# Kernel tuning notes

Hardware: AMD Instinct MI355X
Metric: run time of the kernel (lower is better)

Reference implementation:

```python
import jax, jax.numpy as jnp
import numpy as np

B, N, C, H = 8, 4096, 768, 12
D = C // H  # head dim = 64


def setup_inputs() -> dict:
    key = jax.random.key(0)
    ks = jax.random.split(key, 8)
    s = 1.0 / np.sqrt(C)
    return {
        "q": jax.random.normal(ks[0], (B, N, C), jnp.float32),
        "k": jax.random.normal(ks[1], (B, N, C), jnp.float32),
        "v": jax.random.normal(ks[2], (B, N, C), jnp.float32),
        "Wq": jax.random.normal(ks[3], (C, C), jnp.float32) * s,
        "Wk": jax.random.normal(ks[4], (C, C), jnp.float32) * s,
        "Wv": jax.random.normal(ks[5], (C, C), jnp.float32) * s,
        "Wp": jax.random.normal(ks[6], (C, C), jnp.float32) * s,
        "bp": jax.random.normal(ks[7], (C,), jnp.float32) * 0.01,
    }


def reference(q, k, v, Wq, Wk, Wv, Wp, bp):
    Bq, Nq, Cq = q.shape
    # Linear projections (torch Linear: x @ W.T), no bias (qkv_bias=False)
    qh = (q @ Wq.T).reshape(Bq, Nq, H, D).transpose(0, 2, 1, 3)  # b h n d
    kh = (k @ Wk.T).reshape(Bq, Nq, H, D).transpose(0, 2, 1, 3)
    vh = (v @ Wv.T).reshape(Bq, Nq, H, D).transpose(0, 2, 1, 3)
    # softmax over sequence dim (n)
    k_softmax = jax.nn.softmax(kh, axis=2)
    # context: [b, h, d_k, d_v]
    ctx = jnp.einsum("bhnk,bhnv->bhkv", k_softmax, vh)
    # factorized attention (note: original code never applies self.scale)
    factor_att = jnp.einsum("bhnk,bhkv->bhnv", qh, ctx)
    x = factor_att.transpose(0, 2, 1, 3).reshape(Bq, Nq, Cq)
    # output projection (with bias); dropouts are p=0 -> identity
    return x @ Wp.T + bp
```

## Files before the change

### kernel.cpp

```cpp
#include <hip/hip_runtime.h>
#include <hip/hip_bf16.h>


typedef __bf16 bf16x8 __attribute__((ext_vector_type(8)));
typedef __bf16 bf16x4 __attribute__((ext_vector_type(4)));
typedef float f32x4 __attribute__((ext_vector_type(4)));

#define GLOAD_LDS16(g, l)                                                        \
  __builtin_amdgcn_global_load_lds(                                              \
      (const __attribute__((address_space(1))) void*)(g),                        \
      (__attribute__((address_space(3))) void*)(l), 16, 0, 0)

__device__ __forceinline__ float bf2f(__hip_bfloat16 h) { return __bfloat162float(h); }

__global__ void cast_kernel(const float* __restrict__ src,
                            __bf16* __restrict__ dst, long n) {
  long i = ((long)blockIdx.x * blockDim.x + threadIdx.x) * 4;
  if (i + 3 < n) {
    const float4 f = *(const float4*)(src + i);
    bf16x4 u = {(__bf16)f.x, (__bf16)f.y, (__bf16)f.z, (__bf16)f.w};
    *(bf16x4*)(dst + i) = u;
  }
}

__global__ void cast3_kernel(const float* __restrict__ s0, const float* __restrict__ s1,
                             const float* __restrict__ s2,
                             __bf16* __restrict__ d0, __bf16* __restrict__ d1,
                             __bf16* __restrict__ d2) {
  const float* src = blockIdx.y == 0 ? s0 : (blockIdx.y == 1 ? s1 : s2);
  __bf16* dst = blockIdx.y == 0 ? d0 : (blockIdx.y == 1 ? d1 : d2);
  const long i = ((long)blockIdx.x * blockDim.x + threadIdx.x) * 4;
  const float4 f = *(const float4*)(src + i);
  bf16x4 u = {(__bf16)f.x, (__bf16)f.y, (__bf16)f.z, (__bf16)f.w};
  *(bf16x4*)(dst + i) = u;
}

__global__ void transpose_cast(const float* __restrict__ src,
                               __bf16* __restrict__ dst) {
  __shared__ float tile[32][33];
  const int bx = blockIdx.x * 32, by = blockIdx.y * 32;
  const int tx = threadIdx.x, ty = threadIdx.y;
#pragma unroll
  for (int j = 0; j < 32; j += 8)
    tile[ty + j][tx] = src[(long)(bx + ty + j) * 768 + by + tx];
  __syncthreads();
#pragma unroll
  for (int j = 0; j < 32; j += 8)
    dst[(long)(by + ty + j) * 768 + bx + tx] = (__bf16)tile[tx][ty + j];
}

__global__ __launch_bounds__(256, 2)
void gemm_bt(const __bf16* __restrict__ Abase,
             const __bf16* __restrict__ Btbase,
             __bf16* __restrict__ outBbase,
             float* __restrict__ outF,
             const float* __restrict__ bias,
             long sAz, long sBz, long sOz, long sBbatch) {
  constexpr int K = 768;
  const int tid = threadIdx.x;
  const int lane = tid & 63;
  const int w = tid >> 6;
  const int wr = (w >> 1) * 64;
  const int wc = (w & 1) * 64;

  long flat = ((long)blockIdx.z * gridDim.y + blockIdx.y) * gridDim.x + blockIdx.x;
  const long total = (long)gridDim.x * gridDim.y * gridDim.z;
  if ((total & 7) == 0) {
    flat = (flat & 7) * (total >> 3) + (flat >> 3);
  }
  const int bx = (int)(flat % gridDim.x);
  const long rem = flat / gridDim.x;
  const int by = (int)(rem % gridDim.y);
  const int bz = (int)(rem / gridDim.y);

  const int z = bz;
  const int m0 = by * 128;
  const int n0 = bx * 128;

  const __bf16* A = Abase + (long)z * sAz;
  const __bf16* Bt = Btbase + (long)z * sBz + (long)(m0 >> 12) * sBbatch;

  __shared__ __align__(16) __bf16 As[128 * 64];
  __shared__ __align__(16) __bf16 Bs[128 * 64];

  f32x4 acc[4][4] = {};

  const int ro = lane >> 3;
  const int gck = (lane & 7) ^ ro;
  const __bf16* gA = A + (long)(m0 + w * 8 + ro) * K + gck * 8;
  const __bf16* gB = Bt + (long)(n0 + w * 8 + ro) * K + gck * 8;

  const int rsel = lane & 15;
  const int r7 = rsel & 7;
  const int cseg = lane >> 4;

  for (int k0 = 0; k0 < K; k0 += 64) {
#pragma unroll
    for (int p = 0; p < 4; ++p) {
      GLOAD_LDS16(gA + k0 + (long)p * 32 * K, &As[(p * 32 + w * 8) * 64]);
      GLOAD_LDS16(gB + k0 + (long)p * 32 * K, &Bs[(p * 32 + w * 8) * 64]);
    }
    __syncthreads();

#pragma unroll
    for (int kk = 0; kk < 2; ++kk) {
      const int ckl = kk * 4 + cseg;
      bf16x8 af[4], bfr[4];
#pragma unroll
      for (int i = 0; i < 4; ++i) {
        const int rowa = wr + i * 16 + rsel;
        const int rowb = wc + i * 16 + rsel;
        af[i] = *(const bf16x8*)&As[rowa * 64 + ((ckl ^ r7) << 3)];
        bfr[i] = *(const bf16x8*)&Bs[rowb * 64 + ((ckl ^ r7) << 3)];
      }
#pragma unroll
      for (int i = 0; i < 4; ++i)
#pragma unroll
        for (int j = 0; j < 4; ++j)
          acc[i][j] = __builtin_amdgcn_mfma_f32_16x16x32_bf16(af[i], bfr[j], acc[i][j], 0, 0, 0);
    }
    __syncthreads();
  }

  const int r0 = (lane >> 4) * 4;
  if (outF == nullptr) {
    __bf16* outp = outBbase + (long)z * sOz;
#pragma unroll
    for (int i = 0; i < 4; ++i) {
      const int row = m0 + wr + i * 16 + r0;
#pragma unroll
      for (int j = 0; j < 4; ++j) {
        const int col = n0 + wc + j * 16 + rsel;
#pragma unroll
        for (int r = 0; r < 4; ++r)
          outp[(long)(row + r) * 768 + col] = (__bf16)acc[i][j][r];
      }
    }
  } else {
#pragma unroll
    for (int i = 0; i < 4; ++i) {
      const int row = m0 + wr + i * 16 + r0;
#pragma unroll
      for (int j = 0; j < 4; ++j) {
        const int col = n0 + wc + j * 16 + rsel;
        const float bv = bias[col];
#pragma unroll
        for (int r = 0; r < 4; ++r)
          outF[(long)(row + r) * 768 + col] = acc[i][j][r] + bv;
      }
    }
  }
}

__global__ __launch_bounds__(256)
void ctx_partial(const __hip_bfloat16* __restrict__ Kh,
                 const __hip_bfloat16* __restrict__ Vh,
                 float* __restrict__ Upart, float* __restrict__ Spart) {
  const int bh = blockIdx.y, chunk = blockIdx.x;
  const int b = bh / 12, h = bh % 12;
  const int t = threadIdx.x;
  const int rr = t >> 6, d = t & 63;
  const int tdk = (t & 15) * 4, tdv = (t >> 4) * 4;
  __shared__ float ek[4][64];
  __shared__ float vv[4][64];
  __shared__ float sred[256];
  f32x4 U[4] = {};
  float myS = 0.f;
  const long base = ((long)b * 4096 + (long)chunk * 512) * 768 + h * 64 + d;
  for (int r4 = 0; r4 < 128; ++r4) {
    const long off = base + (long)(r4 * 4 + rr) * 768;
    const float e = __expf(bf2f(Kh[off]));
    ek[rr][d] = e;
    myS += e;
    vv[rr][d] = bf2f(Vh[off]);
    __syncthreads();
#pragma unroll
    for (int q = 0; q < 4; ++q) {
      const f32x4 a = *(const f32x4*)&ek[q][tdk];
      const f32x4 vx = *(const f32x4*)&vv[q][tdv];
      U[0] += a[0] * vx;
      U[1] += a[1] * vx;
      U[2] += a[2] * vx;
      U[3] += a[3] * vx;
    }
    __syncthreads();
  }
  float* Ub = Upart + (long)(bh * 8 + chunk) * 4096;
#pragma unroll
  for (int i = 0; i < 4; ++i) *(f32x4*)&Ub[(tdk + i) * 64 + tdv] = U[i];
  sred[t] = myS;
  __syncthreads();
  if (t < 64) {
    const float s = sred[t] + sred[t + 64] + sred[t + 128] + sred[t + 192];
    Spart[(long)(bh * 8 + chunk) * 64 + t] = s;
  }
}

__global__ __launch_bounds__(256)
void ctx_reduce(const float* __restrict__ Upart, const float* __restrict__ Spart,
                float* __restrict__ ctx) {
  const int bh = blockIdx.x;
  const int t = threadIdx.x;
  const int tdk = (t & 15) * 4, tdv = (t >> 4) * 4;
  __shared__ float S[64];
  if (t < 64) {
    float s = 0.f;
#pragma unroll
    for (int c = 0; c < 8; ++c) s += Spart[(long)(bh * 8 + c) * 64 + t];
    S[t] = s;
  }
  __syncthreads();
#pragma unroll
  for (int i = 0; i < 4; ++i) {
    const int dk = tdk + i;
    f32x4 u = {};
#pragma unroll
    for (int c = 0; c < 8; ++c)
      u += *(const f32x4*)&Upart[(long)(bh * 8 + c) * 4096 + dk * 64 + tdv];
    u *= (1.f / S[dk]);
    *(f32x4*)&ctx[(long)bh * 4096 + dk * 64 + tdv] = u;
  }
}

__global__ __launch_bounds__(256, 2)
void gstack(const float* __restrict__ ctx, const float* __restrict__ Wp,
            __bf16* __restrict__ Gt) {
  const int cc = blockIdx.x, h = blockIdx.y, b = blockIdx.z;
  const int t = threadIdx.x, lane = t & 63, w = t >> 6;
  const int co0 = cc * 192;
  __shared__ __align__(16) float wf[192 * 64];

#pragma unroll
  for (int i = 0; i < 12; ++i) {
    const int flat = i * 256 + t;
    const int r = flat >> 4, c4 = flat & 15;
    const f32x4 vsrc = *(const f32x4*)&Wp[(long)(co0 + r) * 768 + h * 64 + c4 * 4];
    *(f32x4*)&wf[r * 64 + c4 * 4] = vsrc;
  }

  f32x4 cx[16];
  const float* crow = ctx + ((long)(b * 12 + h) * 64 + lane) * 64;
#pragma unroll
  for (int j = 0; j < 16; ++j) cx[j] = *(const f32x4*)&crow[j * 4];

  __syncthreads();

  __bf16* gout = Gt + ((long)(b * 768 + co0 + w * 48) * 768) + h * 64 + lane;
  for (int co = 0; co < 48; ++co) {
    const float* wrow = &wf[(w * 48 + co) * 64];
    f32x4 acc = {};
#pragma unroll
    for (int j = 0; j < 16; ++j) acc += cx[j] * *(const f32x4*)&wrow[j * 4];
    const float s = acc[0] + acc[1] + acc[2] + acc[3];
    gout[(long)co * 768] = (__bf16)s;
  }
}

extern "C" void kernel_launch(void* const* d_in, const int* in_sizes, int n_in,
                              void* d_out, int out_size, void* d_ws, size_t ws_size,
                              hipStream_t stream) {
  (void)in_sizes; (void)n_in; (void)out_size; (void)ws_size;
  const float* q = (const float*)d_in[0];
  const float* k = (const float*)d_in[1];
  const float* v = (const float*)d_in[2];
  const float* Wq = (const float*)d_in[3];
  const float* Wk = (const float*)d_in[4];
  const float* Wv = (const float*)d_in[5];
  const float* Wp = (const float*)d_in[6];
  const float* bp = (const float*)d_in[7];
  float* out = (float*)d_out;

  const long XE = 32768L * 768L;
  const long WE = 768L * 768L;

  char* ws = (char*)d_ws;
  __bf16* Kb = (__bf16*)ws;
  __bf16* Vb = Kb + XE;
  __bf16* Qb = Vb + XE;
  __bf16* Khb = Qb + XE;
  __bf16* Vhb = Khb + XE;
  __bf16* Wb = Vhb + XE;
  __bf16* Gt = Wb + 4 * WE;
  __bf16* Mt = Gt + 8 * WE;
  float* Upart = (float*)(Mt + 8 * WE);
  float* Spart = Upart + 96L * 8 * 4096;
  float* ctx = Spart + 96L * 8 * 64;

  cast_kernel<<<576, 256, 0, stream>>>(Wk, Wb + 0 * WE, WE);
  cast_kernel<<<576, 256, 0, stream>>>(Wv, Wb + 1 * WE, WE);
  transpose_cast<<<dim3(24, 24), dim3(32, 8), 0, stream>>>(Wq, Wb + 3 * WE);
  cast3_kernel<<<dim3(24576, 3), 256, 0, stream>>>(k, v, q, Kb, Vb, Qb);

  gemm_bt<<<dim3(6, 256, 2), 256, 0, stream>>>(Kb, Wb, Khb, nullptr, nullptr,
                                               XE, WE, XE, 0);

  ctx_partial<<<dim3(8, 96), 256, 0, stream>>>((const __hip_bfloat16*)Khb,
                                               (const __hip_bfloat16*)Vhb, Upart, Spart);
  ctx_reduce<<<96, 256, 0, stream>>>(Upart, Spart, ctx);

  gstack<<<dim3(4, 12, 8), 256, 0, stream>>>(ctx, Wp, Gt);

  gemm_bt<<<dim3(6, 6, 8), 256, 0, stream>>>(Gt, Wb + 3 * WE, Mt, nullptr,
                                             nullptr, WE, 0, WE, 0);

  gemm_bt<<<dim3(6, 256, 1), 256, 0, stream>>>(Qb, Mt, nullptr, out,
                                               bp, 0, 0, 0, WE);
}
```

Before: 365.0 us.

## Add 256x256-tile GEMM with phased LDS pipeline for large projections

Adds a new 512-thread GEMM kernel computing 256x256 output tiles with 8 waves, double-buffered direct-to-LDS global loads, swizzled LDS reads, and four barrier-separated MFMA phases using s_setprio. It replaces the 128x128-tile kernel for the K/V projection and the final Q·M output GEMM. The larger tile raises arithmetic intensity and overlaps the next tile's loads with compute, at the cost of fewer blocks (768 and 384), higher register and LDS pressure, and hand-tuned vmcnt waits that must match the load ordering exactly.

```diff
diff --git a/kernel.cpp b/kernel.cpp
--- a/kernel.cpp
+++ b/kernel.cpp
@@ -10,6 +10,20 @@
   __builtin_amdgcn_global_load_lds(                                              \
       (const __attribute__((address_space(1))) void*)(g),                        \
       (__attribute__((address_space(3))) void*)(l), 16, 0, 0)
+
+#define PH_SYNC1                                                                 \
+  do {                                                                           \
+    __builtin_amdgcn_sched_barrier(0);                                           \
+    __builtin_amdgcn_s_barrier();                                                \
+    asm volatile("s_waitcnt lgkmcnt(0)" ::: "memory");                           \
+    __builtin_amdgcn_sched_barrier(0);                                           \
+  } while (0)
+#define PH_SYNC2                                                                 \
+  do {                                                                           \
+    __builtin_amdgcn_sched_barrier(0);                                           \
+    __builtin_amdgcn_s_barrier();                                                \
+    __builtin_amdgcn_sched_barrier(0);                                           \
+  } while (0)
 
 __device__ __forceinline__ float bf2f(__hip_bfloat16 h) { return __bfloat162float(h); }
 
@@ -47,6 +61,187 @@
 #pragma unroll
   for (int j = 0; j < 32; j += 8)
     dst[(long)(by + ty + j) * 768 + bx + tx] = (__bf16)tile[tx][ty + j];
+}
+
+__global__ __launch_bounds__(512, 2)
+void gemm256(const __bf16* __restrict__ Abase,
+             const __bf16* __restrict__ Btbase,
+             __bf16* __restrict__ outBbase,
+             float* __restrict__ outF,
+             const float* __restrict__ bias,
+             long sAz, long sBz, long sOz, long sBbatch) {
+  constexpr int K = 768;
+  const int tid = threadIdx.x;
+  const int lane = tid & 63;
+  const int w = tid >> 6;
+  const int wrow = w >> 2;
+  const int wcol = w & 3;
+
+  long flat = ((long)blockIdx.z * gridDim.y + blockIdx.y) * gridDim.x + blockIdx.x;
+  const long total = (long)gridDim.x * gridDim.y * gridDim.z;
+  if ((total & 7) == 0) {
+    flat = (flat & 7) * (total >> 3) + (flat >> 3);
+  }
+  const int bx = (int)(flat % gridDim.x);
+  const long rem = flat / gridDim.x;
+  const int by = (int)(rem % gridDim.y);
+  const int bz = (int)(rem / gridDim.y);
+
+  const int z = bz;
+  const int m0 = by * 256;
+  const int n0 = bx * 256;
+
+  const __bf16* A = Abase + (long)z * sAz;
+  const __bf16* Bt = Btbase + (long)z * sBz + (long)(m0 >> 12) * sBbatch;
+
+  __shared__ __align__(16) __bf16 ldsA[2][2][128 * 64];
+  __shared__ __align__(16) __bf16 ldsB[2][2][128 * 64];
+
+  f32x4 acc[8][4] = {};
+
+  const int ro = lane >> 3;
+  const int gck = (lane & 7) ^ ro;
+  const __bf16* gA = A + (long)(m0 + w * 8 + ro) * K + gck * 8;
+  const __bf16* gB = Bt + (long)(n0 + w * 8 + ro) * K + gck * 8;
+
+  auto SA = [&](int dd, int hh, int t) {
+#pragma unroll
+    for (int j = 0; j < 2; ++j)
+      GLOAD_LDS16(gA + (long)(hh * 128 + j * 64) * K + t * 64,
+                  &ldsA[dd][hh][(j * 64 + w * 8) * 64]);
+  };
+  auto SB = [&](int dd, int hh, int t) {
+#pragma unroll
+    for (int j = 0; j < 2; ++j)
+      GLOAD_LDS16(gB + (long)(hh * 128 + j * 64) * K + t * 64,
+                  &ldsB[dd][hh][(j * 64 + w * 8) * 64]);
+  };
+
+  const int rsel = lane & 15;
+  const int ck = lane >> 4;
+  const int brow0 = (wcol & 1) * 64;
+
+  SB(0, 0, 0); SB(0, 1, 0); SA(0, 0, 0); SA(0, 1, 0);
+  SB(1, 0, 1); SB(1, 1, 1); SA(1, 0, 1);
+  asm volatile("s_waitcnt vmcnt(6)" ::: "memory");
+  PH_SYNC2;
+
+#pragma unroll 1
+  for (int u = 0; u < 12; ++u) {
+    const int d = u & 1, dn = d ^ 1;
+    const __bf16* Ah = &ldsA[d][wrow][0];
+    const __bf16* Bh = &ldsB[d][wcol >> 1][0];
+    bf16x8 af[8], bf01[4], bf23[4];
+
+#pragma unroll
+    for (int j = 0; j < 4; ++j) {
+      const int row = j * 16 + rsel, sw = row & 7;
+      af[j * 2 + 0] = *(const bf16x8*)&Ah[row * 64 + ((ck ^ sw) << 3)];
+      af[j * 2 + 1] = *(const bf16x8*)&Ah[row * 64 + (((4 + ck) ^ sw) << 3)];
+    }
+#pragma unroll
+    for (int n = 0; n < 2; ++n) {
+      const int row = brow0 + n * 16 + rsel, sw = row & 7;
+      bf01[n * 2 + 0] = *(const bf16x8*)&Bh[row * 64 + ((ck ^ sw) << 3)];
+      bf01[n * 2 + 1] = *(const bf16x8*)&Bh[row * 64 + (((4 + ck) ^ sw) << 3)];
+    }
+    if (u + 1 < 12) SA(dn, 1, u + 1);
+    PH_SYNC1;
+    __builtin_amdgcn_s_setprio(1);
+#pragma unroll
+    for (int j = 0; j < 4; ++j)
+#pragma unroll
+      for (int n = 0; n < 2; ++n) {
+        acc[j][n] = __builtin_amdgcn_mfma_f32_16x16x32_bf16(af[j * 2 + 0], bf01[n * 2 + 0], acc[j][n], 0, 0, 0);
+        acc[j][n] = __builtin_amdgcn_mfma_f32_16x16x32_bf16(af[j * 2 + 1], bf01[n * 2 + 1], acc[j][n], 0, 0, 0);
+      }
+    __builtin_amdgcn_s_setprio(0);
+    PH_SYNC2;
+
+#pragma unroll
+    for (int n = 0; n < 2; ++n) {
+      const int row = brow0 + (2 + n) * 16 + rsel, sw = row & 7;
+      bf23[n * 2 + 0] = *(const bf16x8*)&Bh[row * 64 + ((ck ^ sw) << 3)];
+      bf23[n * 2 + 1] = *(const bf16x8*)&Bh[row * 64 + (((4 + ck) ^ sw) << 3)];
+    }
+    PH_SYNC1;
+    __builtin_amdgcn_s_setprio(1);
+#pragma unroll
+    for (int j = 0; j < 4; ++j)
+#pragma unroll
+      for (int n = 0; n < 2; ++n) {
+        acc[j][2 + n] = __builtin_amdgcn_mfma_f32_16x16x32_bf16(af[j * 2 + 0], bf23[n * 2 + 0], acc[j][2 + n], 0, 0, 0);
+        acc[j][2 + n] = __builtin_amdgcn_mfma_f32_16x16x32_bf16(af[j * 2 + 1], bf23[n * 2 + 1], acc[j][2 + n], 0, 0, 0);
+      }
+    __builtin_amdgcn_s_setprio(0);
+    PH_SYNC2;
+
+#pragma unroll
+    for (int j = 0; j < 4; ++j) {
+      const int row = (4 + j) * 16 + rsel, sw = row & 7;
+      af[j * 2 + 0] = *(const bf16x8*)&Ah[row * 64 + ((ck ^ sw) << 3)];
+      af[j * 2 + 1] = *(const bf16x8*)&Ah[row * 64 + (((4 + ck) ^ sw) << 3)];
+    }
+    if (u + 2 < 12) SB(d, 0, u + 2);
+    PH_SYNC1;
+    __builtin_amdgcn_s_setprio(1);
+#pragma unroll
+    for (int j = 0; j < 4; ++j)
+#pragma unroll
+      for (int n = 0; n < 2; ++n) {
+        acc[4 + j][n] = __builtin_amdgcn_mfma_f32_16x16x32_bf16(af[j * 2 + 0], bf01[n * 2 + 0], acc[4 + j][n], 0, 0, 0);
+        acc[4 + j][n] = __builtin_amdgcn_mfma_f32_16x16x32_bf16(af[j * 2 + 1], bf01[n * 2 + 1], acc[4 + j][n], 0, 0, 0);
+      }
+    __builtin_amdgcn_s_setprio(0);
+    PH_SYNC2;
+
+    if (u + 2 < 12) { SB(d, 1, u + 2); SA(d, 0, u + 2); }
+    if (u <= 9) {
+      asm volatile("s_waitcnt vmcnt(6)" ::: "memory");
+    } else if (u == 10) {
+      asm volatile("s_waitcnt vmcnt(0)" ::: "memory");
+    }
+    PH_SYNC1;
+    __builtin_amdgcn_s_setprio(1);
+#pragma unroll
+    for (int j = 0; j < 4; ++j)
+#pragma unroll
+      for (int n = 0; n < 2; ++n) {
+        acc[4 + j][2 + n] = __builtin_amdgcn_mfma_f32_16x16x32_bf16(af[j * 2 + 0], bf23[n * 2 + 0], acc[4 + j][2 + n], 0, 0, 0);
+        acc[4 + j][2 + n] = __builtin_amdgcn_mfma_f32_16x16x32_bf16(af[j * 2 + 1], bf23[n * 2 + 1], acc[4 + j][2 + n], 0, 0, 0);
+      }
+    __builtin_amdgcn_s_setprio(0);
+    PH_SYNC2;
+  }
+
+  const int r0 = (lane >> 4) * 4;
+  if (outF == nullptr) {
+    __bf16* outp = outBbase + (long)z * sOz;
+#pragma unroll
+    for (int i = 0; i < 8; ++i) {
+      const int row = m0 + wrow * 128 + i * 16 + r0;
+#pragma unroll
+      for (int j = 0; j < 4; ++j) {
+        const int col = n0 + wcol * 64 + j * 16 + rsel;
+#pragma unroll
+        for (int r = 0; r < 4; ++r)
+          outp[(long)(row + r) * 768 + col] = (__bf16)acc[i][j][r];
+      }
+    }
+  } else {
+#pragma unroll
+    for (int i = 0; i < 8; ++i) {
+      const int row = m0 + wrow * 128 + i * 16 + r0;
+#pragma unroll
+      for (int j = 0; j < 4; ++j) {
+        const int col = n0 + wcol * 64 + j * 16 + rsel;
+        const float bv = bias[col];
+#pragma unroll
+        for (int r = 0; r < 4; ++r)
+          outF[(long)(row + r) * 768 + col] = acc[i][j][r] + bv;
+      }
+    }
+  }
 }
 
 __global__ __launch_bounds__(256, 2)
@@ -291,7 +486,7 @@
   transpose_cast<<<dim3(24, 24), dim3(32, 8), 0, stream>>>(Wq, Wb + 3 * WE);
   cast3_kernel<<<dim3(24576, 3), 256, 0, stream>>>(k, v, q, Kb, Vb, Qb);
 
-  gemm_bt<<<dim3(6, 256, 2), 256, 0, stream>>>(Kb, Wb, Khb, nullptr, nullptr,
+  gemm256<<<dim3(3, 128, 2), 512, 0, stream>>>(Kb, Wb, Khb, nullptr, nullptr,
                                                XE, WE, XE, 0);
 
   ctx_partial<<<dim3(8, 96), 256, 0, stream>>>((const __hip_bfloat16*)Khb,
@@ -303,6 +498,6 @@
   gemm_bt<<<dim3(6, 6, 8), 256, 0, stream>>>(Gt, Wb + 3 * WE, Mt, nullptr,
                                              nullptr, WE, 0, WE, 0);
 
-  gemm_bt<<<dim3(6, 256, 1), 256, 0, stream>>>(Qb, Mt, nullptr, out,
+  gemm256<<<dim3(3, 128, 1), 512, 0, stream>>>(Qb, Mt, nullptr, out,
                                                bp, 0, 0, 0, WE);
 }
```

After: 372.1 us. Within noise of the previous version (+1.9%).

## Fuse fp32-to-bf16 activation cast into GEMM A-tile loads and batch ctx reduction

Applied to the files above, without the earlier changes.

Removes the separate cast kernel for q, k and v. The GEMMs now read fp32 activations straight into LDS and convert them to bf16 while building the MFMA operand fragments. This drops a full pass that wrote and reread bf16 copies of all three inputs, at the price of twice the A-tile LDS footprint and extra conversion work in the inner loop. The ctx_partial kernel is also restructured to load 32 rows per iteration with vectorised bf16x8 loads, which means fewer barriers per row.

```diff
diff --git a/kernel.cpp b/kernel.cpp
--- a/kernel.cpp
+++ b/kernel.cpp
@@ -23,18 +23,6 @@
   }
 }
 
-__global__ void cast3_kernel(const float* __restrict__ s0, const float* __restrict__ s1,
-                             const float* __restrict__ s2,
-                             __bf16* __restrict__ d0, __bf16* __restrict__ d1,
-                             __bf16* __restrict__ d2) {
-  const float* src = blockIdx.y == 0 ? s0 : (blockIdx.y == 1 ? s1 : s2);
-  __bf16* dst = blockIdx.y == 0 ? d0 : (blockIdx.y == 1 ? d1 : d2);
-  const long i = ((long)blockIdx.x * blockDim.x + threadIdx.x) * 4;
-  const float4 f = *(const float4*)(src + i);
-  bf16x4 u = {(__bf16)f.x, (__bf16)f.y, (__bf16)f.z, (__bf16)f.w};
-  *(bf16x4*)(dst + i) = u;
-}
-
 __global__ void transpose_cast(const float* __restrict__ src,
                                __bf16* __restrict__ dst) {
   __shared__ float tile[32][33];
@@ -49,8 +37,9 @@
     dst[(long)(by + ty + j) * 768 + bx + tx] = (__bf16)tile[tx][ty + j];
 }
 
+template <bool AF32>
 __global__ __launch_bounds__(256, 2)
-void gemm_bt(const __bf16* __restrict__ Abase,
+void gemm_bt(const void* __restrict__ Abase_, const void* __restrict__ A2,
              const __bf16* __restrict__ Btbase,
              __bf16* __restrict__ outBbase,
              float* __restrict__ outF,
@@ -77,40 +66,70 @@
   const int m0 = by * 128;
   const int n0 = bx * 128;
 
-  const __bf16* A = Abase + (long)z * sAz;
   const __bf16* Bt = Btbase + (long)z * sBz + (long)(m0 >> 12) * sBbatch;
 
-  __shared__ __align__(16) __bf16 As[128 * 64];
+  __shared__ __align__(16) float AsF[AF32 ? 128 * 64 : 8];
+  __shared__ __align__(16) __bf16 AsB[AF32 ? 8 : 128 * 64];
   __shared__ __align__(16) __bf16 Bs[128 * 64];
 
   f32x4 acc[4][4] = {};
 
   const int ro = lane >> 3;
   const int gck = (lane & 7) ^ ro;
-  const __bf16* gA = A + (long)(m0 + w * 8 + ro) * K + gck * 8;
   const __bf16* gB = Bt + (long)(n0 + w * 8 + ro) * K + gck * 8;
+
+  const void* Asel = (A2 != nullptr && z == 1) ? A2 : Abase_;
+  const long az = (A2 == nullptr) ? (long)z * sAz : 0;
+  const float* gAf = nullptr;
+  const __bf16* gAb = nullptr;
+  if constexpr (AF32) {
+    const int arow = tid >> 4;
+    const int ach = (tid & 15) ^ arow;
+    gAf = (const float*)Asel + az + (long)(m0 + arow) * K + ach * 4;
+  } else {
+    gAb = (const __bf16*)Asel + az + (long)(m0 + w * 8 + ro) * K + gck * 8;
+  }
 
   const int rsel = lane & 15;
   const int r7 = rsel & 7;
   const int cseg = lane >> 4;
 
   for (int k0 = 0; k0 < K; k0 += 64) {
-#pragma unroll
-    for (int p = 0; p < 4; ++p) {
-      GLOAD_LDS16(gA + k0 + (long)p * 32 * K, &As[(p * 32 + w * 8) * 64]);
-      GLOAD_LDS16(gB + k0 + (long)p * 32 * K, &Bs[(p * 32 + w * 8) * 64]);
+    if constexpr (AF32) {
+#pragma unroll
+      for (int p = 0; p < 8; ++p)
+        GLOAD_LDS16(gAf + k0 + (long)p * 16 * K, &AsF[p * 1024 + w * 256]);
+#pragma unroll
+      for (int p = 0; p < 4; ++p)
+        GLOAD_LDS16(gB + k0 + (long)p * 32 * K, &Bs[(p * 32 + w * 8) * 64]);
+    } else {
+#pragma unroll
+      for (int p = 0; p < 4; ++p) {
+        GLOAD_LDS16(gAb + k0 + (long)p * 32 * K, &AsB[(p * 32 + w * 8) * 64]);
+        GLOAD_LDS16(gB + k0 + (long)p * 32 * K, &Bs[(p * 32 + w * 8) * 64]);
+      }
     }
     __syncthreads();
 
 #pragma unroll
     for (int kk = 0; kk < 2; ++kk) {
-      const int ckl = kk * 4 + cseg;
       bf16x8 af[4], bfr[4];
 #pragma unroll
       for (int i = 0; i < 4; ++i) {
         const int rowa = wr + i * 16 + rsel;
         const int rowb = wc + i * 16 + rsel;
-        af[i] = *(const bf16x8*)&As[rowa * 64 + ((ckl ^ r7) << 3)];
+        if constexpr (AF32) {
+          const int c0 = kk * 8 + cseg * 2;
+          const f32x4 lo = *(const f32x4*)&AsF[rowa * 64 + ((c0 ^ rsel) << 2)];
+          const f32x4 hi = *(const f32x4*)&AsF[rowa * 64 + (((c0 + 1) ^ rsel) << 2)];
+          bf16x8 a = {(__bf16)lo[0], (__bf16)lo[1], (__bf16)lo[2], (__bf16)lo[3],
+                      (__bf16)hi[0], (__bf16)hi[1], (__bf16)hi[2], (__bf16)hi[3]};
+          af[i] = a;
+        } else {
+          const int ckl = kk * 4 + cseg;
+          af[i] = *(const bf16x8*)&AsB[rowa * 64 + ((ckl ^ r7) << 3)];
+        }
+        const int ckl = kk * 4 + cseg;
         bfr[i] = *(const bf16x8*)&Bs[rowb * 64 + ((ckl ^ r7) << 3)];
       }
 #pragma unroll
@@ -153,47 +172,49 @@
 }
 
 __global__ __launch_bounds__(256)
-void ctx_partial(const __hip_bfloat16* __restrict__ Kh,
-                 const __hip_bfloat16* __restrict__ Vh,
+void ctx_partial(const __bf16* __restrict__ Kh,
+                 const __bf16* __restrict__ Vh,
                  float* __restrict__ Upart, float* __restrict__ Spart) {
   const int bh = blockIdx.y, chunk = blockIdx.x;
   const int b = bh / 12, h = bh % 12;
   const int t = threadIdx.x;
-  const int rr = t >> 6, d = t & 63;
   const int tdk = (t & 15) * 4, tdv = (t >> 4) * 4;
-  __shared__ float ek[4][64];
-  __shared__ float vv[4][64];
-  __shared__ float sred[256];
+  const int sr = t >> 3, sc = (t & 7) * 8;
+  __shared__ float ek[32][64];
+  __shared__ float vv[32][64];
   f32x4 U[4] = {};
-  float myS = 0.f;
-  const long base = ((long)b * 4096 + (long)chunk * 512) * 768 + h * 64 + d;
-  for (int r4 = 0; r4 < 128; ++r4) {
-    const long off = base + (long)(r4 * 4 + rr) * 768;
-    const float e = __expf(bf2f(Kh[off]));
-    ek[rr][d] = e;
-    myS += e;
-    vv[rr][d] = bf2f(Vh[off]);
+  float sacc = 0.f;
+  const long base = ((long)b * 4096 + (long)chunk * 512) * 768 + h * 64;
+#pragma unroll 1
+  for (int it = 0; it < 16; ++it) {
+    const long roff = base + (long)(it * 32 + sr) * 768 + sc;
+    const bf16x8 kb = *(const bf16x8*)(Kh + roff);
+    const bf16x8 vb = *(const bf16x8*)(Vh + roff);
     __syncthreads();
 #pragma unroll
-    for (int q = 0; q < 4; ++q) {
-      const f32x4 a = *(const f32x4*)&ek[q][tdk];
-      const f32x4 vx = *(const f32x4*)&vv[q][tdv];
+    for (int j = 0; j < 8; ++j) {
+      ek[sr][sc + j] = __expf((float)kb[j]);
+      vv[sr][sc + j] = (float)vb[j];
+    }
+    __syncthreads();
+#pragma unroll 4
+    for (int r = 0; r < 32; ++r) {
+      const f32x4 a = *(const f32x4*)&ek[r][tdk];
+      const f32x4 vx = *(const f32x4*)&vv[r][tdv];
       U[0] += a[0] * vx;
       U[1] += a[1] * vx;
       U[2] += a[2] * vx;
       U[3] += a[3] * vx;
     }
-    __syncthreads();
+    if (t < 64) {
+#pragma unroll 4
+      for (int r = 0; r < 32; ++r) sacc += ek[r][t];
+    }
   }
   float* Ub = Upart + (long)(bh * 8 + chunk) * 4096;
 #pragma unroll
   for (int i = 0; i < 4; ++i) *(f32x4*)&Ub[(tdk + i) * 64 + tdv] = U[i];
-  sred[t] = myS;
-  __syncthreads();
-  if (t < 64) {
-    const float s = sred[t] + sred[t + 64] + sred[t + 128] + sred[t + 192];
-    Spart[(long)(bh * 8 + chunk) * 64 + t] = s;
-  }
+  if (t < 64) Spart[(long)(bh * 8 + chunk) * 64 + t] = sacc;
 }
 
 __global__ __launch_bounds__(256)
@@ -274,10 +295,7 @@
   const long WE = 768L * 768L;
 
   char* ws = (char*)d_ws;
-  __bf16* Kb = (__bf16*)ws;
-  __bf16* Vb = Kb + XE;
-  __bf16* Qb = Vb + XE;
-  __bf16* Khb = Qb + XE;
+  __bf16* Khb = (__bf16*)ws;
   __bf16* Vhb = Khb + XE;
   __bf16* Wb = Vhb + XE;
   __bf16* Gt = Wb + 4 * WE;
@@ -289,20 +307,18 @@
   cast_kernel<<<576, 256, 0, stream>>>(Wk, Wb + 0 * WE, WE);
   cast_kernel<<<576, 256, 0, stream>>>(Wv, Wb + 1 * WE, WE);
   transpose_cast<<<dim3(24, 24), dim3(32, 8), 0, stream>>>(Wq, Wb + 3 * WE);
-  cast3_kernel<<<dim3(24576, 3), 256, 0, stream>>>(k, v, q, Kb, Vb, Qb);
-
-  gemm_bt<<<dim3(6, 256, 2), 256, 0, stream>>>(Kb, Wb, Khb, nullptr, nullptr,
-                                               XE, WE, XE, 0);
-
-  ctx_partial<<<dim3(8, 96), 256, 0, stream>>>((const __hip_bfloat16*)Khb,
-                                               (const __hip_bfloat16*)Vhb, Upart, Spart);
+
+  gemm_bt<true><<<dim3(6, 256, 2), 256, 0, stream>>>(k, v, Wb, Khb, nullptr,
+                                                     nullptr, 0, WE, XE, 0);
+
+  ctx_partial<<<dim3(8, 96), 256, 0, stream>>>(Khb, Vhb, Upart, Spart);
   ctx_reduce<<<96, 256, 0, stream>>>(Upart, Spart, ctx);
 
   gstack<<<dim3(4, 12, 8), 256, 0, stream>>>(ctx, Wp, Gt);
 
-  gemm_bt<<<dim3(6, 6, 8), 256, 0, stream>>>(Gt, Wb + 3 * WE, Mt, nullptr,
-                                             nullptr, WE, 0, WE, 0);
-
-  gemm_bt<<<dim3(6, 256, 1), 256, 0, stream>>>(Qb, Mt, nullptr, out,
-                                               bp, 0, 0, 0, WE);
-}
+  gemm_bt<false><<<dim3(6, 6, 8), 256, 0, stream>>>(Gt, nullptr, Wb + 3 * WE, Mt,
+                                                    nullptr, nullptr, WE, 0, WE, 0);
+
+  gemm_bt<true><<<dim3(6, 256, 1), 256, 0, stream>>>(q, nullptr, Mt, nullptr, out,
+                                                     bp, 0, 0, 0, WE);
+}
```

After: 299.7 us. 1.22x faster.
